# Performance work log

Measured on AMD Instinct MI355X. Metric: run time of the kernel, lower is better.

## Reference

```python
import jax, jax.numpy as jnp
import numpy as np
from jax import lax

B, N, NPOINT, NSAMPLE = 16, 8192, 2048, 32
RADIUS = 0.45
D_FEAT = 64
MLP = (64, 64, 128)
EPS = 1e-5  # BatchNorm2d default eps


def setup_inputs() -> dict:
    key = jax.random.key(0)
    ks = jax.random.split(key, 8)
    inp = {
        "xyz": jax.random.uniform(ks[0], (B, 3, N), dtype=jnp.float32),
        "points": jax.random.normal(ks[1], (B, D_FEAT, N), dtype=jnp.float32),
    }
    dims = (3 + D_FEAT,) + MLP
    for i in range(len(MLP)):
        ci, co = dims[i], dims[i + 1]
        inp[f"W{i}"] = jax.random.normal(ks[2 + i], (co, ci), dtype=jnp.float32) / np.float32(np.sqrt(ci))
        inp[f"b{i}"] = jnp.zeros((co,), jnp.float32)
        inp[f"gamma{i}"] = jnp.ones((co,), jnp.float32)
        inp[f"beta{i}"] = jnp.zeros((co,), jnp.float32)
    return inp


def _fps(xyz_t, npoint):
    # farthest point sampling; xyz_t: [B, N, 3] -> [B, npoint] indices
    Bc, Nc, _ = xyz_t.shape

    def step(carry, _):
        distance, farthest = carry
        centroid = jnp.take_along_axis(xyz_t, farthest[:, None, None], axis=1)  # [B,1,3]
        d = jnp.sum((xyz_t - centroid) ** 2, axis=-1)  # [B,N]
        distance = jnp.minimum(distance, d)
        return (distance, jnp.argmax(distance, axis=-1)), farthest

    init = (jnp.full((Bc, Nc), 1e10, xyz_t.dtype), jnp.zeros((Bc,), jnp.int32))
    _, cents = lax.scan(step, init, None, length=npoint)
    return jnp.transpose(cents)  # [B, npoint]


def _gather(pts, idx):
    # pts: [B, N, C], idx: [B, ...] -> [B, ..., C]
    return jax.vmap(lambda p, i: p[i])(pts, idx)


def _forward(xyz, points, params):
    xyz_t = jnp.transpose(xyz, (0, 2, 1))     # [B,N,3]
    pts_t = jnp.transpose(points, (0, 2, 1))  # [B,N,D]

    fps_idx = _fps(xyz_t, NPOINT)
    new_xyz = _gather(xyz_t, fps_idx)         # [B,S,3]

    # ball query -- faithful to source: Euclidean DISTANCE compared vs radius**2
    d2 = (jnp.sum(new_xyz ** 2, -1)[:, :, None]
          + jnp.sum(xyz_t ** 2, -1)[:, None, :]
          - 2.0 * jnp.einsum('bsc,bnc->bsn', new_xyz, xyz_t))
    dist = jnp.sqrt(jnp.maximum(d2, 0.0))     # [B,S,N] == torch.cdist
    neg_vals, idx = lax.top_k(-dist, NSAMPLE)
    group_idx = jnp.where(-neg_vals < RADIUS ** 2, idx, 0)  # [B,S,K]

    grouped_xyz = _gather(xyz_t, group_idx) - new_xyz[:, :, None, :]  # [B,S,K,3]
    grouped_pts = _gather(pts_t, group_idx)                           # [B,S,K,D]
    feats = jnp.concatenate([grouped_xyz, grouped_pts], axis=-1)      # [B,S,K,3+D]

    # shared MLP: 1x1 conv + BatchNorm (training-mode batch stats) + ReLU
    for (W, b, g, be) in params:
        h = jnp.einsum('bskc,oc->bsko', feats, W) + b
        mean = jnp.mean(h, axis=(0, 1, 2))
        var = jnp.var(h, axis=(0, 1, 2))  # biased, like torch BN normalization
        feats = jax.nn.relu(g * (h - mean) * lax.rsqrt(var + EPS) + be)

    new_points = jnp.max(feats, axis=2)  # max over nsample -> [B,S,C_out]
    return jnp.transpose(new_xyz, (0, 2, 1)), jnp.transpose(new_points, (0, 2, 1))


def reference(xyz, points, W0, b0, gamma0, beta0, W1, b1, gamma1, beta1, W2, b2, gamma2, beta2):
    params = [(W0, b0, gamma0, beta0), (W1, b1, gamma1, beta1), (W2, b2, gamma2, beta2)]
    return _forward(xyz, points, params)
```

## Files before the change

kernel.cpp:

```cpp
#include <hip/hip_runtime.h>

#define B_ 16
#define N_ 8192
#define S_ 2048
#define K_ 32
#define EPSBN 1e-5
#define CAP 1024

#define OFF_PARTA    0ul
#define OFF_NEWXYZ   131072ul
#define OFF_GIDX     524288ul
#define OFF_Q1       4718592ul
#define OFF_C1       38273024ul
#define OFF_PART     46661632ul
#define OFF_AFF1     55050240ul
#define OFF_AFF2     55051264ul
#define OFF_AFF3     55052288ul
#define OFF_H3MAX    55053312ul
#define OFF_H3MIN    71830528ul

#define STG(row, c) ((row)*33 + ((row)>>5) + (c))

template<int CTRL, int RM>
__device__ __forceinline__ unsigned long long dppmove(unsigned long long x) {
    unsigned int lo = (unsigned int)x, hi = (unsigned int)(x >> 32);
    unsigned int lo2 = (unsigned int)__builtin_amdgcn_update_dpp((int)lo, (int)lo, CTRL, RM, 0xf, false);
    unsigned int hi2 = (unsigned int)__builtin_amdgcn_update_dpp((int)hi, (int)hi, CTRL, RM, 0xf, false);
    return ((unsigned long long)hi2 << 32) | lo2;
}
__device__ __forceinline__ unsigned long long wave_max_u64(unsigned long long x) {
    unsigned long long t;
    t = dppmove<0x111, 0xf>(x); x = (t > x) ? t : x;
    t = dppmove<0x112, 0xf>(x); x = (t > x) ? t : x;
    t = dppmove<0x114, 0xf>(x); x = (t > x) ? t : x;
    t = dppmove<0x118, 0xf>(x); x = (t > x) ? t : x;
    t = dppmove<0x142, 0xa>(x); x = (t > x) ? t : x;
    t = dppmove<0x143, 0xc>(x); x = (t > x) ? t : x;
    return x;
}
__device__ __forceinline__ unsigned long long wave_min_u64(unsigned long long x) {
    unsigned long long t;
    t = dppmove<0x111, 0xf>(x); x = (t < x) ? t : x;
    t = dppmove<0x112, 0xf>(x); x = (t < x) ? t : x;
    t = dppmove<0x114, 0xf>(x); x = (t < x) ? t : x;
    t = dppmove<0x118, 0xf>(x); x = (t < x) ? t : x;
    t = dppmove<0x142, 0xa>(x); x = (t < x) ? t : x;
    t = dppmove<0x143, 0xc>(x); x = (t < x) ? t : x;
    return x;
}

__global__ __launch_bounds__(512) void fps_kernel(const float* __restrict__ xyz,
                                                  const float* __restrict__ pts,
                                                  const float* __restrict__ W0,
                                                  const float* __restrict__ b0,
                                                  float* __restrict__ Q1,
                                                  float* __restrict__ nxyz,
                                                  float* __restrict__ out0) {
    __shared__ float xs[N_], ys[N_], zs[N_];
    __shared__ int farHist[S_];
    __shared__ unsigned long long kq[2][4];
    int tid = threadIdx.x;
    if (blockIdx.x >= 16) {
        int o = tid & 63, jj = tid >> 6;
        int blk = blockIdx.x - 16;
        int b = blk >> 10;
        int j = ((blk & 1023) << 3) + jj;
        const float* xb = xyz + (size_t)b * 3 * N_;
        const float* pb = pts + (size_t)b * 64 * N_;
        float acc = b0[o];
#pragma unroll
        for (int c = 0; c < 3; c++) acc += W0[o * 67 + c] * xb[c * N_ + j];
#pragma unroll 8
        for (int c = 0; c < 64; c++) acc += W0[o * 67 + 3 + c] * pb[c * N_ + j];
        Q1[(((size_t)b << 13) + j) * 64 + o] = acc;
        return;
    }
    int b = blockIdx.x;
    const float* xb = xyz + (size_t)b * 3 * N_;
    for (int i = tid; i < N_; i += 512) {
        xs[i] = xb[i]; ys[i] = xb[N_ + i]; zs[i] = xb[2 * N_ + i];
    }
    __syncthreads();
    float px[32], py[32], pz[32], d8[32];
    if (tid < 256) {
#pragma unroll
        for (int k = 0; k < 32; k++) {
            int i = tid + k * 256;
            px[k] = xs[i]; py[k] = ys[i]; pz[k] = zs[i];
            d8[k] = 1e10f;
        }
    }
    int far = 0;
    int w = tid >> 6;
    for (int t = 0; t < S_; t++) {
        if (tid < 256) {
            if (tid == 0) farHist[t] = far;
            float cx = xs[far], cy = ys[far], cz = zs[far];
            float bv = -1.f; int bk = 0;
#pragma unroll
            for (int k = 0; k < 32; k++) {
                float dx = px[k] - cx, dy = py[k] - cy, dz = pz[k] - cz;
                float d = dx * dx + dy * dy + dz * dz;
                float dd = fminf(d8[k], d); d8[k] = dd;
                if (dd > bv) { bv = dd; bk = k; }
            }
            int bi = tid + bk * 256;
            unsigned long long kk = (((unsigned long long)__float_as_uint(bv)) << 32)
                                  | (unsigned)(8191 - bi);
            kk = wave_max_u64(kk);
            if ((tid & 63) == 63) kq[t & 1][w] = kk;
        }
        __syncthreads();
        if (tid < 256) {
            int buf = t & 1;
            unsigned long long fk = kq[buf][0];
#pragma unroll
            for (int q = 1; q < 4; q++) { unsigned long long o = kq[buf][q]; fk = (o > fk) ? o : fk; }
            far = 8191 - (int)(fk & 0xffffffffull);
        }
    }
    __syncthreads();
    for (int s = tid; s < S_; s += 512) {
        int idx = farHist[s];
        float x = xs[idx], y = ys[idx], z = zs[idx];
        int g = b * S_ + s;
        nxyz[g * 3 + 0] = x; nxyz[g * 3 + 1] = y; nxyz[g * 3 + 2] = z;
        out0[(b * 3 + 0) * S_ + s] = x;
        out0[(b * 3 + 1) * S_ + s] = y;
        out0[(b * 3 + 2) * S_ + s] = z;
    }
}

__global__ __launch_bounds__(64) void ball_kernel(const float* __restrict__ xyz,
                                                  const float* __restrict__ nxyz,
                                                  int* __restrict__ gidx) {
    __shared__ unsigned long long keys[CAP];
    __shared__ int cnt;
    int bs = blockIdx.x; int b = bs >> 11; int tid = threadIdx.x;
    const float* xb = xyz + (size_t)b * 3 * N_;
    float cx = nxyz[bs * 3 + 0], cy = nxyz[bs * 3 + 1], cz = nxyz[bs * 3 + 2];
    float csq = __fadd_rn(__fadd_rn(__fmul_rn(cx, cx), __fmul_rn(cy, cy)), __fmul_rn(cz, cz));
    const float R2F = (float)(0.45 * 0.45);
    if (tid == 0) cnt = 0;
    __syncthreads();
    for (int j = tid; j < N_; j += 64) {
        float qx = xb[j], qy = xb[N_ + j], qz = xb[2 * N_ + j];
        float psq = __fadd_rn(__fadd_rn(__fmul_rn(qx, qx), __fmul_rn(qy, qy)), __fmul_rn(qz, qz));
        float t = __fmul_rn(cx, qx);
        t = __fmaf_rn(cy, qy, t);
        t = __fmaf_rn(cz, qz, t);
        float d2 = __fsub_rn(__fadd_rn(csq, psq), __fadd_rn(t, t));
        float dist = __fsqrt_rn(fmaxf(d2, 0.0f));
        if (dist < R2F) {
            int p = atomicAdd(&cnt, 1);
            if (p < CAP) keys[p] = (((unsigned long long)__float_as_uint(dist)) << 32) | (unsigned)j;
        }
    }
    __syncthreads();
    int nc = cnt; if (nc > CAP) nc = CAP;
    for (int k = 0; k < K_; k++) {
        unsigned long long bk = ~0ull;
        for (int i = tid; i < nc; i += 64) {
            unsigned long long kv = keys[i];
            bk = (kv < bk) ? kv : bk;
        }
        bk = wave_min_u64(bk);
        unsigned int lo = (unsigned int)__builtin_amdgcn_readlane((int)(unsigned int)bk, 63);
        unsigned int hi = (unsigned int)__builtin_amdgcn_readlane((int)(unsigned int)(bk >> 32), 63);
        unsigned long long mk = ((unsigned long long)hi << 32) | lo;
        int j = 0;
        if (mk != ~0ull) {
            j = (int)(mk & 0xffffffffull);
            for (int i = tid; i < nc; i += 64)
                if (keys[i] == mk) keys[i] = ~0ull;
        }
        if (tid == 0) gidx[bs * K_ + k] = j;
    }
}

__global__ __launch_bounds__(256) void c1_kernel(const float* __restrict__ nxyz,
                                                 const float* __restrict__ W0,
                                                 float* __restrict__ C1) {
    int tid = threadIdx.x; int o = tid & 63, ss = tid >> 6;
    int gs = blockIdx.x * 4 + ss;
    float acc = 0.f;
#pragma unroll
    for (int c = 0; c < 3; c++) acc += W0[o * 67 + c] * nxyz[gs * 3 + c];
    C1[(size_t)gs * 64 + o] = acc;
}

__global__ __launch_bounds__(256) void stats1_kernel(const float* __restrict__ Q1,
                                                     const float* __restrict__ C1,
                                                     const int* __restrict__ gidx,
                                                     double* __restrict__ part) {
    __shared__ double ds1[4][64], ds2[4][64];
    int tid = threadIdx.x; int o = tid & 63, ll = tid >> 6;
    double s1 = 0, s2 = 0;
    for (int it = 0; it < 256; it++) {
        int slot = it * 4096 + blockIdx.x * 4 + ll;
        int b = slot >> 16; int r = slot & 65535; int s = r >> 5;
        int g = gidx[slot];
        float q = Q1[(((size_t)b << 13) + g) * 64 + o];
        float c = C1[((size_t)(b << 11) + s) * 64 + o];
        float h = q - c;
        s1 += h; s2 += (double)h * (double)h;
    }
    ds1[ll][o] = s1; ds2[ll][o] = s2;
    __syncthreads();
    if (tid < 64) {
        double a = 0, bb = 0;
        for (int l = 0; l < 4; l++) { a += ds1[l][tid]; bb += ds2[l][tid]; }
        part[blockIdx.x * 256 + tid * 2] = a;
        part[blockIdx.x * 256 + tid * 2 + 1] = bb;
    }
}

__global__ void stats_reduceA_kernel(const double* __restrict__ part, int nblocks,
                                     double* __restrict__ partA) {
    int per = nblocks >> 6;
    int a = blockIdx.x;
    int c = threadIdx.x;
    double s = 0;
    for (int k = 0; k < per; k++)
        s += part[((size_t)(a * per + k)) * 256 + c];
    partA[(size_t)a * 256 + c] = s;
}

__global__ void stats_reduce_kernel(const double* __restrict__ part, int nblocks, int C,
                                    const float* __restrict__ gamma, const float* __restrict__ beta,
                                    float* __restrict__ aff) {
    __shared__ double s1s[512], s2s[512];
    int tid = threadIdx.x;
    int q = tid / C; int o = tid - q * C;
    double s1 = 0, s2 = 0;
    for (int i = q; i < nblocks; i += 4) {
        s1 += part[(size_t)i * 256 + o * 2];
        s2 += part[(size_t)i * 256 + o * 2 + 1];
    }
    s1s[tid] = s1; s2s[tid] = s2;
    __syncthreads();
    if (tid < C) {
        double a1 = s1s[tid] + s1s[tid + C] + s1s[tid + 2 * C] + s1s[tid + 3 * C];
        double a2 = s2s[tid] + s2s[tid + C] + s2s[tid + 2 * C] + s2s[tid + 3 * C];
        const double cnt = 1048576.0;
        double mean = a1 / cnt;
        double var = a2 / cnt - mean * mean; if (var < 0) var = 0;
        double a = (double)gamma[tid] / sqrt(var + EPSBN);
        double c = (double)beta[tid] - a * mean;
        aff[tid] = (float)a; aff[C + tid] = (float)c;
    }
}

__global__ __launch_bounds__(256) void layer2_stats_kernel(const float* __restrict__ Q1,
                                                           const float* __restrict__ C1,
                                                           const int* __restrict__ gidx,
                                                           const float* __restrict__ aff1,
                                                           const float* __restrict__ W1,
                                                           const float* __restrict__ b1,
                                                           double* __restrict__ part) {
    __shared__ __align__(16) float Wl[64 * 64];
    __shared__ float stage[256 * 33 + 8];
    __shared__ float sA[64], sC[64], sB[64];
    __shared__ double r1[8][33], r2[8][33];
    int tid = threadIdx.x;
    for (int i = tid; i < 4096; i += 256) { int o = i >> 6, c = i & 63; Wl[c * 64 + o] = W1[i]; }
    if (tid < 64) { sA[tid] = aff1[tid]; sC[tid] = aff1[64 + tid]; sB[tid] = b1[tid]; }
    __syncthreads();
    int slot = blockIdx.x * 256 + tid;
    int b = slot >> 16; int r = slot & 65535; int s = r >> 5;
    int g = gidx[slot];
    float x[64];
    {
        const float4* qp4 = (const float4*)(Q1 + (((size_t)b << 13) + g) * 64);
        const float4* cp4 = (const float4*)(C1 + ((size_t)(b << 11) + s) * 64);
#pragma unroll
        for (int c4 = 0; c4 < 16; c4++) {
            float4 q = qp4[c4], cc = cp4[c4];
            int c = c4 * 4;
            x[c + 0] = fmaxf(0.f, sA[c + 0] * (q.x - cc.x) + sC[c + 0]);
            x[c + 1] = fmaxf(0.f, sA[c + 1] * (q.y - cc.y) + sC[c + 1]);
            x[c + 2] = fmaxf(0.f, sA[c + 2] * (q.z - cc.z) + sC[c + 2]);
            x[c + 3] = fmaxf(0.f, sA[c + 3] * (q.w - cc.w) + sC[c + 3]);
        }
    }
    const float4* Wl4 = (const float4*)Wl;
    for (int ch = 0; ch < 2; ch++) {
        float acc[32];
#pragma unroll
        for (int o = 0; o < 32; o++) acc[o] = sB[ch * 32 + o];
#pragma unroll
        for (int c = 0; c < 64; c++) {
            float xv = x[c];
#pragma unroll
            for (int og = 0; og < 8; og++) {
                float4 w = Wl4[c * 16 + ch * 8 + og];
                acc[og * 4 + 0] += w.x * xv; acc[og * 4 + 1] += w.y * xv;
                acc[og * 4 + 2] += w.z * xv; acc[og * 4 + 3] += w.w * xv;
            }
        }
#pragma unroll
        for (int o = 0; o < 32; o++) stage[STG(tid, o)] = acc[o];
        __syncthreads();
        int chn = tid & 31, rr = tid >> 5;
        double s1 = 0, s2 = 0;
        for (int row = rr * 32; row < rr * 32 + 32; row++) {
            float v = stage[STG(row, chn)];
            s1 += v; s2 += (double)v * (double)v;
        }
        r1[rr][chn] = s1; r2[rr][chn] = s2;
        __syncthreads();
        if (tid < 32) {
            double a = 0, bb = 0;
            for (int l = 0; l < 8; l++) { a += r1[l][tid]; bb += r2[l][tid]; }
            part[blockIdx.x * 256 + (ch * 32 + tid) * 2] = a;
            part[blockIdx.x * 256 + (ch * 32 + tid) * 2 + 1] = bb;
        }
        __syncthreads();
    }
}

__global__ __launch_bounds__(256) void layer3_kernel(const float* __restrict__ Q1,
                                                     const float* __restrict__ C1,
                                                     const int* __restrict__ gidx,
                                                     const float* __restrict__ aff1,
                                                     const float* __restrict__ aff2,
                                                     const float* __restrict__ W1,
                                                     const float* __restrict__ b1,
                                                     const float* __restrict__ W2,
                                                     const float* __restrict__ b2,
                                                     double* __restrict__ part,
                                                     float* __restrict__ h3max,
                                                     float* __restrict__ h3min) {
    __shared__ __align__(16) float Wl[64 * 128];
    __shared__ float stage[256 * 33 + 8];
    __shared__ float sA1[64], sC1[64], sB1[64], sA2[64], sC2[64], sB2[128];
    __shared__ double r1[8][33], r2[8][33];
    int tid = threadIdx.x;
    for (int i = tid; i < 4096; i += 256) { int o = i >> 6, c = i & 63; Wl[c * 64 + o] = W1[i]; }
    if (tid < 64) {
        sA1[tid] = aff1[tid]; sC1[tid] = aff1[64 + tid]; sB1[tid] = b1[tid];
        sA2[tid] = aff2[tid]; sC2[tid] = aff2[64 + tid];
    }
    __syncthreads();
    int slot = blockIdx.x * 256 + tid;
    int b = slot >> 16; int r = slot & 65535; int s = r >> 5;
    int g = gidx[slot];
    float x[64];
    {
        const float4* qp4 = (const float4*)(Q1 + (((size_t)b << 13) + g) * 64);
        const float4* cp4 = (const float4*)(C1 + ((size_t)(b << 11) + s) * 64);
#pragma unroll
        for (int c4 = 0; c4 < 16; c4++) {
            float4 q = qp4[c4], cc = cp4[c4];
            int c = c4 * 4;
            x[c + 0] = fmaxf(0.f, sA1[c + 0] * (q.x - cc.x) + sC1[c + 0]);
            x[c + 1] = fmaxf(0.f, sA1[c + 1] * (q.y - cc.y) + sC1[c + 1]);
            x[c + 2] = fmaxf(0.f, sA1[c + 2] * (q.z - cc.z) + sC1[c + 2]);
            x[c + 3] = fmaxf(0.f, sA1[c + 3] * (q.w - cc.w) + sC1[c + 3]);
        }
    }
    const float4* Wl4 = (const float4*)Wl;
    float x3[64];
    for (int ch = 0; ch < 2; ch++) {
        float acc[32];
#pragma unroll
        for (int o = 0; o < 32; o++) acc[o] = sB1[ch * 32 + o];
#pragma unroll
        for (int c = 0; c < 64; c++) {
            float xv = x[c];
#pragma unroll
            for (int og = 0; og < 8; og++) {
                float4 w = Wl4[c * 16 + ch * 8 + og];
                acc[og * 4 + 0] += w.x * xv; acc[og * 4 + 1] += w.y * xv;
                acc[og * 4 + 2] += w.z * xv; acc[og * 4 + 3] += w.w * xv;
            }
        }
#pragma unroll
        for (int o = 0; o < 32; o++) {
            int oo = ch * 32 + o;
            x3[oo] = fmaxf(0.f, sA2[oo] * acc[o] + sC2[oo]);
        }
    }
    __syncthreads();
    for (int i = tid; i < 8192; i += 256) { int o = i >> 6, c = i & 63; Wl[c * 128 + o] = W2[i]; }
    if (tid < 128) sB2[tid] = b2[tid];
    __syncthreads();
    for (int ch = 0; ch < 4; ch++) {
        float acc[32];
#pragma unroll
        for (int o = 0; o < 32; o++) acc[o] = sB2[ch * 32 + o];
#pragma unroll
        for (int c = 0; c < 64; c++) {
            float xv = x3[c];
#pragma unroll
            for (int og = 0; og < 8; og++) {
                float4 w = Wl4[c * 32 + ch * 8 + og];
                acc[og * 4 + 0] += w.x * xv; acc[og * 4 + 1] += w.y * xv;
                acc[og * 4 + 2] += w.z * xv; acc[og * 4 + 3] += w.w * xv;
            }
        }
#pragma unroll
        for (int o = 0; o < 32; o++) stage[STG(tid, o)] = acc[o];
        __syncthreads();
        int chn = tid & 31, rr = tid >> 5;
        double s1 = 0, s2 = 0;
        float mx = -3.402823466e38f, mn = 3.402823466e38f;
        for (int row = rr * 32; row < rr * 32 + 32; row++) {
            float v = stage[STG(row, chn)];
            s1 += v; s2 += (double)v * (double)v;
            mx = fmaxf(mx, v); mn = fminf(mn, v);
        }
        r1[rr][chn] = s1; r2[rr][chn] = s2;
        int gg = blockIdx.x * 8 + rr;
        int bb_ = gg >> 11, ss_ = gg & 2047;
        h3max[((size_t)bb_ * 128 + ch * 32 + chn) * 2048 + ss_] = mx;
        h3min[((size_t)bb_ * 128 + ch * 32 + chn) * 2048 + ss_] = mn;
        __syncthreads();
        if (tid < 32) {
            double a = 0, bb = 0;
            for (int l = 0; l < 8; l++) { a += r1[l][tid]; bb += r2[l][tid]; }
            part[blockIdx.x * 256 + (ch * 32 + tid) * 2] = a;
            part[blockIdx.x * 256 + (ch * 32 + tid) * 2 + 1] = bb;
        }
        __syncthreads();
    }
}

__global__ void final_kernel(const float* __restrict__ h3max, const float* __restrict__ h3min,
                             const float* __restrict__ aff3, float* __restrict__ out1) {
    int idx = blockIdx.x * 256 + threadIdx.x;
    int ch = (idx >> 11) & 127;
    float a = aff3[ch], cv = aff3[128 + ch];
    float v = (a >= 0.f) ? h3max[idx] : h3min[idx];
    out1[idx] = fmaxf(0.f, a * v + cv);
}

extern "C" void kernel_launch(void* const* d_in, const int* in_sizes, int n_in,
                              void* d_out, int out_size, void* d_ws, size_t ws_size,
                              hipStream_t stream) {
    (void)in_sizes; (void)n_in; (void)out_size; (void)ws_size;
    const float* xyz = (const float*)d_in[0];
    const float* pts = (const float*)d_in[1];
    const float* W0  = (const float*)d_in[2];
    const float* b0  = (const float*)d_in[3];
    const float* g0  = (const float*)d_in[4];
    const float* be0 = (const float*)d_in[5];
    const float* W1  = (const float*)d_in[6];
    const float* b1  = (const float*)d_in[7];
    const float* g1  = (const float*)d_in[8];
    const float* be1 = (const float*)d_in[9];
    const float* W2  = (const float*)d_in[10];
    const float* b2  = (const float*)d_in[11];
    const float* g2  = (const float*)d_in[12];
    const float* be2 = (const float*)d_in[13];

    char* ws = (char*)d_ws;
    double* partA  = (double*)(ws + OFF_PARTA);
    float*  nxyz   = (float*)(ws + OFF_NEWXYZ);
    int*    gidx   = (int*)(ws + OFF_GIDX);
    float*  Q1     = (float*)(ws + OFF_Q1);
    float*  C1b    = (float*)(ws + OFF_C1);
    double* part   = (double*)(ws + OFF_PART);
    float*  aff1   = (float*)(ws + OFF_AFF1);
    float*  aff2   = (float*)(ws + OFF_AFF2);
    float*  aff3   = (float*)(ws + OFF_AFF3);
    float*  h3mx   = (float*)(ws + OFF_H3MAX);
    float*  h3mn   = (float*)(ws + OFF_H3MIN);
    float*  out0   = (float*)d_out;
    float*  out1   = out0 + B_ * 3 * S_;

    fps_kernel<<<16 + 16384, 512, 0, stream>>>(xyz, pts, W0, b0, Q1, nxyz, out0);
    ball_kernel<<<B_ * S_, 64, 0, stream>>>(xyz, nxyz, gidx);
    c1_kernel<<<(B_ * S_) / 4, 256, 0, stream>>>(nxyz, W0, C1b);
    stats1_kernel<<<1024, 256, 0, stream>>>(Q1, C1b, gidx, part);
    stats_reduceA_kernel<<<64, 256, 0, stream>>>(part, 1024, partA);
    stats_reduce_kernel<<<1, 256, 0, stream>>>(partA, 64, 64, g0, be0, aff1);
    layer2_stats_kernel<<<4096, 256, 0, stream>>>(Q1, C1b, gidx, aff1, W1, b1, part);
    stats_reduceA_kernel<<<64, 256, 0, stream>>>(part, 4096, partA);
    stats_reduce_kernel<<<1, 256, 0, stream>>>(partA, 64, 64, g1, be1, aff2);
    layer3_kernel<<<4096, 256, 0, stream>>>(Q1, C1b, gidx, aff1, aff2, W1, b1, W2, b2,
                                            part, h3mx, h3mn);
    stats_reduceA_kernel<<<64, 256, 0, stream>>>(part, 4096, partA);
    stats_reduce_kernel<<<1, 512, 0, stream>>>(partA, 64, 128, g2, be2, aff3);
    final_kernel<<<(B_ * 128 * S_) / 256, 256, 0, stream>>>(h3mx, h3mn, aff3, out1);
}
```

Baseline: 3.506 ms.

## Materialize layer-2 pre-activations to skip recomputing them in layer 3

Layer 2 now writes its pre-BN outputs (64 channels per grouped slot, 256 MB) to a workspace buffer, and a new layer-3 kernel reads them back instead of regathering Q1/C1 and recomputing the layer-1 and layer-2 GEMMs. This trades recomputation of the 64x64 matmul and a random gather for an extra 256 MB write and a 256 MB streaming read. The path is only taken when the workspace is large enough; otherwise the old recompute kernel runs.

```diff
diff --git a/kernel.cpp b/kernel.cpp
--- a/kernel.cpp
+++ b/kernel.cpp
@@ -18,6 +18,8 @@
 #define OFF_AFF3     55052288ul
 #define OFF_H3MAX    55053312ul
 #define OFF_H3MIN    71830528ul
+#define OFF_H2       88607744ul
+#define WS_NEED_H2   (OFF_H2 + 268435456ul)
 
 #define STG(row, c) ((row)*33 + ((row)>>5) + (c))
 
@@ -257,7 +259,8 @@
                                                            const float* __restrict__ aff1,
                                                            const float* __restrict__ W1,
                                                            const float* __restrict__ b1,
-                                                           double* __restrict__ part) {
+                                                           double* __restrict__ part,
+                                                           float* __restrict__ h2out) {
     __shared__ __align__(16) float Wl[64 * 64];
     __shared__ float stage[256 * 33 + 8];
     __shared__ float sA[64], sC[64], sB[64];
@@ -297,6 +300,12 @@
                 acc[og * 4 + 0] += w.x * xv; acc[og * 4 + 1] += w.y * xv;
                 acc[og * 4 + 2] += w.z * xv; acc[og * 4 + 3] += w.w * xv;
             }
+        }
+        if (h2out) {
+            float4* o4 = (float4*)(h2out + (size_t)slot * 64 + ch * 32);
+#pragma unroll
+            for (int og = 0; og < 8; og++)
+                o4[og] = make_float4(acc[og * 4 + 0], acc[og * 4 + 1], acc[og * 4 + 2], acc[og * 4 + 3]);
         }
 #pragma unroll
         for (int o = 0; o < 32; o++) stage[STG(tid, o)] = acc[o];
@@ -426,6 +435,78 @@
     }
 }
 
+__global__ __launch_bounds__(256) void layer3_fast_kernel(const float* __restrict__ h2in,
+                                                          const float* __restrict__ aff2,
+                                                          const float* __restrict__ W2,
+                                                          const float* __restrict__ b2,
+                                                          double* __restrict__ part,
+                                                          float* __restrict__ h3max,
+                                                          float* __restrict__ h3min) {
+    __shared__ __align__(16) float Wl[64 * 128];
+    __shared__ float stage[256 * 33 + 8];
+    __shared__ float sA2[64], sC2[64], sB2[128];
+    __shared__ double r1[8][33], r2[8][33];
+    int tid = threadIdx.x;
+    for (int i = tid; i < 8192; i += 256) { int o = i >> 6, c = i & 63; Wl[c * 128 + o] = W2[i]; }
+    if (tid < 64) { sA2[tid] = aff2[tid]; sC2[tid] = aff2[64 + tid]; }
+    if (tid < 128) sB2[tid] = b2[tid];
+    __syncthreads();
+    int slot = blockIdx.x * 256 + tid;
+    float x3[64];
+    {
+        const float4* h4 = (const float4*)(h2in + (size_t)slot * 64);
+#pragma unroll
+        for (int c4 = 0; c4 < 16; c4++) {
+            float4 h = h4[c4];
+            int c = c4 * 4;
+            x3[c + 0] = fmaxf(0.f, sA2[c + 0] * h.x + sC2[c + 0]);
+            x3[c + 1] = fmaxf(0.f, sA2[c + 1] * h.y + sC2[c + 1]);
+            x3[c + 2] = fmaxf(0.f, sA2[c + 2] * h.z + sC2[c + 2]);
+            x3[c + 3] = fmaxf(0.f, sA2[c + 3] * h.w + sC2[c + 3]);
+        }
+    }
+    const float4* Wl4 = (const float4*)Wl;
+    for (int ch = 0; ch < 4; ch++) {
+        float acc[32];
+#pragma unroll
+        for (int o = 0; o < 32; o++) acc[o] = sB2[ch * 32 + o];
+#pragma unroll
+        for (int c = 0; c < 64; c++) {
+            float xv = x3[c];
+#pragma unroll
+            for (int og = 0; og < 8; og++) {
+                float4 w = Wl4[c * 32 + ch * 8 + og];
+                acc[og * 4 + 0] += w.x * xv; acc[og * 4 + 1] += w.y * xv;
+                acc[og * 4 + 2] += w.z * xv; acc[og * 4 + 3] += w.w * xv;
+            }
+        }
+#pragma unroll
+        for (int o = 0; o < 32; o++) stage[STG(tid, o)] = acc[o];
+        __syncthreads();
+        int chn = tid & 31, rr = tid >> 5;
+        double s1 = 0, s2 = 0;
+        float mx = -3.402823466e38f, mn = 3.402823466e38f;
+        for (int row = rr * 32; row < rr * 32 + 32; row++) {
+            float v = stage[STG(row, chn)];
+            s1 += v; s2 += (double)v * (double)v;
+            mx = fmaxf(mx, v); mn = fminf(mn, v);
+        }
+        r1[rr][chn] = s1; r2[rr][chn] = s2;
+        int gg = blockIdx.x * 8 + rr;
+        int bb_ = gg >> 11, ss_ = gg & 2047;
+        h3max[((size_t)bb_ * 128 + ch * 32 + chn) * 2048 + ss_] = mx;
+        h3min[((size_t)bb_ * 128 + ch * 32 + chn) * 2048 + ss_] = mn;
+        __syncthreads();
+        if (tid < 32) {
+            double a = 0, bb = 0;
+            for (int l = 0; l < 8; l++) { a += r1[l][tid]; bb += r2[l][tid]; }
+            part[blockIdx.x * 256 + (ch * 32 + tid) * 2] = a;
+            part[blockIdx.x * 256 + (ch * 32 + tid) * 2 + 1] = bb;
+        }
+        __syncthreads();
+    }
+}
+
 __global__ void final_kernel(const float* __restrict__ h3max, const float* __restrict__ h3min,
                              const float* __restrict__ aff3, float* __restrict__ out1) {
     int idx = blockIdx.x * 256 + threadIdx.x;
@@ -438,7 +519,7 @@
 extern "C" void kernel_launch(void* const* d_in, const int* in_sizes, int n_in,
                               void* d_out, int out_size, void* d_ws, size_t ws_size,
                               hipStream_t stream) {
-    (void)in_sizes; (void)n_in; (void)out_size; (void)ws_size;
+    (void)in_sizes; (void)n_in; (void)out_size;
     const float* xyz = (const float*)d_in[0];
     const float* pts = (const float*)d_in[1];
     const float* W0  = (const float*)d_in[2];
@@ -469,17 +550,24 @@
     float*  out0   = (float*)d_out;
     float*  out1   = out0 + B_ * 3 * S_;
 
+    bool useH2 = ws_size >= WS_NEED_H2;
+    float* h2buf = useH2 ? (float*)(ws + OFF_H2) : (float*)0;
+
     fps_kernel<<<16 + 16384, 512, 0, stream>>>(xyz, pts, W0, b0, Q1, nxyz, out0);
     ball_kernel<<<B_ * S_, 64, 0, stream>>>(xyz, nxyz, gidx);
     c1_kernel<<<(B_ * S_) / 4, 256, 0, stream>>>(nxyz, W0, C1b);
     stats1_kernel<<<1024, 256, 0, stream>>>(Q1, C1b, gidx, part);
     stats_reduceA_kernel<<<64, 256, 0, stream>>>(part, 1024, partA);
     stats_reduce_kernel<<<1, 256, 0, stream>>>(partA, 64, 64, g0, be0, aff1);
-    layer2_stats_kernel<<<4096, 256, 0, stream>>>(Q1, C1b, gidx, aff1, W1, b1, part);
+    layer2_stats_kernel<<<4096, 256, 0, stream>>>(Q1, C1b, gidx, aff1, W1, b1, part, h2buf);
     stats_reduceA_kernel<<<64, 256, 0, stream>>>(part, 4096, partA);
     stats_reduce_kernel<<<1, 256, 0, stream>>>(partA, 64, 64, g1, be1, aff2);
-    layer3_kernel<<<4096, 256, 0, stream>>>(Q1, C1b, gidx, aff1, aff2, W1, b1, W2, b2,
-                                            part, h3mx, h3mn);
+    if (useH2) {
+        layer3_fast_kernel<<<4096, 256, 0, stream>>>(h2buf, aff2, W2, b2, part, h3mx, h3mn);
+    } else {
+        layer3_kernel<<<4096, 256, 0, stream>>>(Q1, C1b, gidx, aff1, aff2, W1, b1, W2, b2,
+                                                part, h3mx, h3mn);
+    }
     stats_reduceA_kernel<<<64, 256, 0, stream>>>(part, 4096, partA);
     stats_reduce_kernel<<<1, 512, 0, stream>>>(partA, 64, 128, g2, be2, aff3);
     final_kernel<<<(B_ * 128 * S_) / 256, 256, 0, stream>>>(h3mx, h3mn, aff3, out1);
```

Measured after the change: 3.591 ms. 2.4% more time.
